# Optimization experiments

Hardware: AMD Instinct MI355X
Metric: run time of the kernel (lower is better)

Reference implementation:

```python
import jax, jax.numpy as jnp
import numpy as np

DIM = 4096
N_HEADS = 32
N_KV_HEADS = 8
HEAD_DIM = 128
ROPE_BASE = 10000.0
B, L = 4, 1024
NEG_INF = -1e9


def rope_traditional(x, base=ROPE_BASE, offset=0):
    # x: [B, H, L, Dh]; rotates interleaved pairs (x[...,2i], x[...,2i+1])
    Dh = x.shape[-1]
    Lx = x.shape[2]
    inv_freq = base ** (-jnp.arange(0, Dh, 2, dtype=jnp.float32) / Dh)  # [Dh/2]
    pos = jnp.arange(offset, offset + Lx, dtype=jnp.float32)
    ang = pos[:, None] * inv_freq  # [L, Dh/2]
    cos, sin = jnp.cos(ang), jnp.sin(ang)
    x1, x2 = x[..., ::2], x[..., 1::2]
    r1 = x1 * cos - x2 * sin
    r2 = x1 * sin + x2 * cos
    return jnp.stack([r1, r2], axis=-1).reshape(x.shape).astype(x.dtype)


def setup_inputs() -> dict:
    key = jax.random.key(0)
    ks = jax.random.split(key, 5)
    x = jax.random.normal(ks[0], (B, L, DIM), dtype=jnp.float32)
    # additive causal mask: 0 on/below diag, -inf-like above
    mask = jnp.where(jnp.tril(jnp.ones((L, L), dtype=bool)), 0.0, NEG_INF).astype(jnp.float32)
    wq = jax.random.normal(ks[1], (DIM, N_HEADS * HEAD_DIM), dtype=jnp.float32) * 0.02
    wk = jax.random.normal(ks[2], (DIM, N_KV_HEADS * HEAD_DIM), dtype=jnp.float32) * 0.02
    wv = jax.random.normal(ks[3], (DIM, N_KV_HEADS * HEAD_DIM), dtype=jnp.float32) * 0.02
    wo = jax.random.normal(ks[4], (N_HEADS * HEAD_DIM, DIM), dtype=jnp.float32) * 0.02
    return {"x": x, "mask": mask, "wq": wq, "wk": wk, "wv": wv, "wo": wo}


def reference(x, mask, wq, wk, wv, wo):
    Bx, Lx, D = x.shape
    scale = HEAD_DIM ** -0.5
    repeats = N_HEADS // N_KV_HEADS
    q = (x @ wq).reshape(Bx, Lx, N_HEADS, HEAD_DIM).transpose(0, 2, 1, 3)      # [B,H,L,Dh]
    k = (x @ wk).reshape(Bx, Lx, N_KV_HEADS, HEAD_DIM).transpose(0, 2, 1, 3)   # [B,Hkv,L,Dh]
    v = (x @ wv).reshape(Bx, Lx, N_KV_HEADS, HEAD_DIM).transpose(0, 2, 1, 3)
    # GQA expansion: head h attends to kv head h % n_kv_heads (matches
    # expand_dims+repeat(axis=1)+reshape in the original)
    k = jnp.tile(k, (1, repeats, 1, 1))  # [B,H,L,Dh]
    v = jnp.tile(v, (1, repeats, 1, 1))
    # cache=None path: rope with offset 0
    q = rope_traditional(q)
    k = rope_traditional(k)
    scores = jnp.einsum("bhqd,bhkd->bhqk", q * scale, k) + mask
    probs = jax.nn.softmax(scores.astype(jnp.float32), axis=-1).astype(scores.dtype)
    out = jnp.einsum("bhqk,bhkd->bhqd", probs, v)
    out = out.transpose(0, 2, 1, 3).reshape(Bx, Lx, D)
    return out @ wo
```

## Files before the change

kernel.cpp:

```cpp
#include <hip/hip_runtime.h>
#include <stdint.h>

typedef unsigned short u16;
typedef __bf16 bf16x8 __attribute__((ext_vector_type(8)));
typedef float f32x4 __attribute__((ext_vector_type(4)));

__device__ __forceinline__ u16 f2b(float x) {
  uint32_t b = __float_as_uint(x);
  b += 0x7fff + ((b >> 16) & 1);
  return (u16)(b >> 16);
}
__device__ __forceinline__ float b2f(u16 u) {
  return __uint_as_float(((uint32_t)u) << 16);
}

#define GLD16(src, dst)                                                                  \
  __builtin_amdgcn_global_load_lds((const __attribute__((address_space(1))) void*)(src),\
                                   (__attribute__((address_space(3))) void*)(dst), 16, 0, 0)

__device__ __forceinline__ f32x4 mfma16(bf16x8 a, bf16x8 b, f32x4 c) {
  return __builtin_amdgcn_mfma_f32_16x16x32_bf16(a, b, c, 0, 0, 0);
}

__global__ void k_rope_table(float2* __restrict__ tab) {
  int i = blockIdx.x * 256 + threadIdx.x;
  int l = i >> 6, d = i & 63;
  float inv = powf(10000.0f, -(float)(2 * d) / 128.0f);
  float ang = (float)l * inv;
  float s, c;
  sincosf(ang, &s, &c);
  tab[i] = make_float2(c, s);
}

__global__ void k_cast8(const float* __restrict__ src, u16* __restrict__ dst) {
  size_t i = (size_t)blockIdx.x * 256 + threadIdx.x;
  const float4* s4 = (const float4*)src;
  float4 a = s4[2 * i], b = s4[2 * i + 1];
  union { u16 u[8]; uint4 v; } o;
  o.u[0] = f2b(a.x); o.u[1] = f2b(a.y); o.u[2] = f2b(a.z); o.u[3] = f2b(a.w);
  o.u[4] = f2b(b.x); o.u[5] = f2b(b.y); o.u[6] = f2b(b.z); o.u[7] = f2b(b.w);
  ((uint4*)dst)[i] = o.v;
}

__global__ __launch_bounds__(256) void k_tcast(const float* __restrict__ src,
                                               u16* __restrict__ dst, int R, int C) {
  __shared__ u16 t[64][72];
  int tiles_c = C >> 6;
  int tr = blockIdx.x / tiles_c, tc = blockIdx.x % tiles_c;
  int tid = threadIdx.x;
  {
    int rr = tid >> 4, cv = tid & 15;
#pragma unroll
    for (int it = 0; it < 4; ++it) {
      int row = rr + it * 16;
      float4 v = *(const float4*)(src + (size_t)(tr * 64 + row) * C + tc * 64 + cv * 4);
      t[row][cv * 4 + 0] = f2b(v.x);
      t[row][cv * 4 + 1] = f2b(v.y);
      t[row][cv * 4 + 2] = f2b(v.z);
      t[row][cv * 4 + 3] = f2b(v.w);
    }
  }
  __syncthreads();
  {
    int cc = tid >> 3, g = tid & 7;
#pragma unroll
    for (int it = 0; it < 2; ++it) {
      int c = cc + it * 32;
      union { u16 u[8]; uint4 v; } o;
#pragma unroll
      for (int j = 0; j < 8; ++j) o.u[j] = t[g * 8 + j][c];
      *(uint4*)(dst + (size_t)(tc * 64 + c) * R + tr * 64 + g * 8) = o.v;
    }
  }
}

__global__ __launch_bounds__(256) void k_vtrans(const u16* __restrict__ qkv,
                                                u16* __restrict__ vrt) {
  __shared__ u16 t[64][72];
  int b = blockIdx.x >> 8;
  int tt = blockIdx.x & 255;
  int tr = tt >> 4, tc = tt & 15;
  int tid = threadIdx.x;
  {
    int rr = tid >> 3, g = tid & 7;
#pragma unroll
    for (int it = 0; it < 2; ++it) {
      int row = rr + it * 32;
      union { u16 u[8]; uint4 v; } o;
      o.v = *(const uint4*)(qkv + (size_t)(b * 1024 + tr * 64 + row) * 6144 + 5120 + tc * 64 + g * 8);
#pragma unroll
      for (int j = 0; j < 8; ++j) t[row][g * 8 + j] = o.u[j];
    }
  }
  __syncthreads();
  {
    int cc = tid >> 3, g = tid & 7;
#pragma unroll
    for (int it = 0; it < 2; ++it) {
      int c = cc + it * 32;
      union { u16 u[8]; uint4 v; } o;
#pragma unroll
      for (int j = 0; j < 8; ++j) o.u[j] = t[g * 8 + j][c];
      *(uint4*)(vrt + (size_t)(b * 1024 + tc * 64 + c) * 1024 + tr * 64 + g * 8) = o.v;
    }
  }
}

__global__ void k_rope(const u16* __restrict__ qkv, const float2* __restrict__ tab,
                       u16* __restrict__ qr, u16* __restrict__ kr) {
  int u = blockIdx.x * 256 + threadIdx.x;
  int row = u / 2560;
  int j = u - row * 2560;
  int b = row >> 10, l = row & 1023;
  const float scale = 0.08838834764831845f;
  if (j < 2048) {
    int h = j >> 6, dp = j & 63;
    uint32_t pair = *(const uint32_t*)(qkv + (size_t)row * 6144 + h * 128 + 2 * dp);
    float2 cs = tab[l * 64 + dp];
    float x1 = b2f((u16)pair), x2 = b2f((u16)(pair >> 16));
    float r1 = (x1 * cs.x - x2 * cs.y) * scale;
    float r2 = (x1 * cs.y + x2 * cs.x) * scale;
    uint32_t outw = (uint32_t)f2b(r1) | ((uint32_t)f2b(r2) << 16);
    *(uint32_t*)(qr + ((size_t)((b * 32 + h) * 1024 + l)) * 128 + 2 * dp) = outw;
  } else {
    int jj = j - 2048;
    int kh = jj >> 6, dp = jj & 63;
    uint32_t pair = *(const uint32_t*)(qkv + (size_t)row * 6144 + 4096 + kh * 128 + 2 * dp);
    float2 cs = tab[l * 64 + dp];
    float x1 = b2f((u16)pair), x2 = b2f((u16)(pair >> 16));
    float r1 = x1 * cs.x - x2 * cs.y;
    float r2 = x1 * cs.y + x2 * cs.x;
    uint32_t outw = (uint32_t)f2b(r1) | ((uint32_t)f2b(r2) << 16);
    *(uint32_t*)(kr + ((size_t)((b * 8 + kh) * 1024 + l)) * 128 + 2 * dp) = outw;
  }
}


#define STAGE2(s0, s1, koff, ldsoff)          \
  GLD16((s0) + (koff), dst0 + (ldsoff));      \
  GLD16((s1) + (koff), dst1 + (ldsoff));

#define LOADB(base, kh)                                                   \
  bfr[0] = *(const bf16x8*)((base) + (kh) * 8192 + 0 * 512);              \
  bfr[1] = *(const bf16x8*)((base) + (kh) * 8192 + 1 * 512);              \
  bfr[2] = *(const bf16x8*)((base) + (kh) * 8192 + 2 * 512);              \
  bfr[3] = *(const bf16x8*)((base) + (kh) * 8192 + 3 * 512);

#define LOADA(base, kh, mh)                                               \
  afr[0] = *(const bf16x8*)((base) + (kh) * 8192 + (mh) * 2048 + 0 * 512);\
  afr[1] = *(const bf16x8*)((base) + (kh) * 8192 + (mh) * 2048 + 1 * 512);\
  afr[2] = *(const bf16x8*)((base) + (kh) * 8192 + (mh) * 2048 + 2 * 512);\
  afr[3] = *(const bf16x8*)((base) + (kh) * 8192 + (mh) * 2048 + 3 * 512);

#define PH_TAIL(mh)                                                       \
  __builtin_amdgcn_sched_barrier(0);                                      \
  __builtin_amdgcn_s_barrier();                                           \
  asm volatile("s_waitcnt lgkmcnt(0)" ::: "memory");                      \
  __builtin_amdgcn_sched_barrier(0);                                      \
  __builtin_amdgcn_s_setprio(1);                                          \
  _Pragma("unroll") for (int mm = 0; mm < 4; ++mm)                        \
    _Pragma("unroll") for (int n_ = 0; n_ < 4; ++n_)                      \
      acc[(mh) * 4 + mm][n_] = mfma16(afr[mm], bfr[n_], acc[(mh) * 4 + mm][n_]); \
  __builtin_amdgcn_s_setprio(0);                                          \
  __builtin_amdgcn_sched_barrier(0);                                      \
  __builtin_amdgcn_s_barrier();

template <typename OutT>
__global__ __launch_bounds__(512, 2) void k_gemm8(const u16* __restrict__ A,
                                                  const u16* __restrict__ Bt,
                                                  OutT* __restrict__ C,
                                                  int M, int N, int K) {
  extern __shared__ u16 lds[];
  const int tid = threadIdx.x;
  const int lane = tid & 63, wid = tid >> 6;
  const int l16 = lane & 15, lhi = lane >> 4;
  const int wm = wid >> 2, wn = wid & 3;

  const int nbn = N >> 8;
  int bid = blockIdx.x;
  const int cpx = gridDim.x >> 3;
  bid = (bid & 7) * cpx + (bid >> 3);
  const int bm = (bid / nbn) << 8;
  const int bn = (bid % nbn) << 8;

  const u16* Ag = A + (size_t)bm * K;
  const u16* Bg = Bt + (size_t)bn * K;

  const int swz = (lhi ^ ((l16 >> 1) & 3)) << 3;
  const u16* pA0 = lds + wm * 4096 + l16 * 32 + swz;
  const u16* pA1 = pA0 + 32768;
  const u16* pB0 = lds + 16384 + wn * 2048 + l16 * 32 + swz;
  const u16* pB1 = pB0 + 32768;

  const int r0 = tid >> 2, g0 = tid & 3;
  const int r1 = r0 + 128;
  const size_t so0 = (size_t)r0 * K + ((g0 ^ ((r0 >> 1) & 3)) << 3);
  const size_t so1 = (size_t)r1 * K + ((g0 ^ ((r1 >> 1) & 3)) << 3);
  const u16* sA0 = Ag + so0;
  const u16* sA1 = Ag + so1;
  const u16* sB0 = Bg + so0;
  const u16* sB1 = Bg + so1;
  u16* dst0 = lds + wid * 512;
  u16* dst1 = lds + 4096 + wid * 512;

  f32x4 acc[8][4] = {};
  bf16x8 bfr[4], afr[4];

  STAGE2(sA0, sA1, 0, 0);
  STAGE2(sA0, sA1, 32, 8192);
  STAGE2(sB0, sB1, 0, 16384);
  STAGE2(sB0, sB1, 32, 24576);
  STAGE2(sB0, sB1, 64, 49152);
  STAGE2(sA0, sA1, 64, 32768);
  STAGE2(sB0, sB1, 96, 57344);
  asm volatile("s_waitcnt vmcnt(6)" ::: "memory");
  __builtin_amdgcn_s_barrier();

  const int nt = K >> 6;
  for (int t = 0; t < nt; t += 2) {
    const bool more = (t + 2) < nt;
    const int kA1 = (t + 1) * 64 + 32;
    const int k2 = (t + 2) * 64;
    const int k3 = (t + 3) * 64;
    LOADB(pB0, 0)
    LOADA(pA0, 0, 0)
    STAGE2(sA0, sA1, kA1, 40960);
    PH_TAIL(0)
    LOADA(pA0, 0, 1)
    if (more) { STAGE2(sB0, sB1, k2, 16384); }
    PH_TAIL(1)
    LOADB(pB0, 1)
    LOADA(pA0, 1, 0)
    if (more) { STAGE2(sA0, sA1, k2, 0); }
    PH_TAIL(0)
    LOADA(pA0, 1, 1)
    if (more) {
      STAGE2(sB0, sB1, k2 + 32, 24576);
      asm volatile("s_waitcnt vmcnt(6)" ::: "memory");
    } else {
      asm volatile("s_waitcnt vmcnt(0)" ::: "memory");
    }
    PH_TAIL(1)
    LOADB(pB1, 0)
    LOADA(pA1, 0, 0)
    if (more) { STAGE2(sA0, sA1, k2 + 32, 8192); }
    PH_TAIL(0)
    LOADA(pA1, 0, 1)
    if (more) { STAGE2(sB0, sB1, k3, 49152); }
    PH_TAIL(1)
    LOADB(pB1, 1)
    LOADA(pA1, 1, 0)
    if (more) { STAGE2(sA0, sA1, k3, 32768); }
    PH_TAIL(0)
    LOADA(pA1, 1, 1)
    if (more) {
      STAGE2(sB0, sB1, k3 + 32, 57344);
      asm volatile("s_waitcnt vmcnt(6)" ::: "memory");
    }
    PH_TAIL(1)
  }

#pragma unroll
  for (int m = 0; m < 8; ++m) {
    int row = bm + wm * 128 + m * 16 + lhi * 4;
#pragma unroll
    for (int n = 0; n < 4; ++n) {
      int col = bn + wn * 64 + n * 16 + l16;
#pragma unroll
      for (int r = 0; r < 4; ++r) {
        float v = acc[m][n][r];
        size_t idx = (size_t)(row + r) * N + col;
        if constexpr (sizeof(OutT) == 2) C[idx] = f2b(v);
        else C[idx] = v;
      }
    }
  }
}

__global__ __launch_bounds__(512) void k_attn(const u16* __restrict__ qr,
                                              const u16* __restrict__ kr,
                                              const u16* __restrict__ vrt,
                                              u16* __restrict__ ao) {
  __shared__ u16 Klds[8192];
  __shared__ u16 Vlds[8192];
  __shared__ u16 Plds[9216];
  int bid = blockIdx.x;
  int qb = bid & 7, h = (bid >> 3) & 31, b = bid >> 8;
  int kvh = h & 7;
  int lane = threadIdx.x & 63, w = threadIdx.x >> 6;
  int l16 = lane & 15, lhi = lane >> 4;
  int qmin = qb * 128 + w * 16;

  const u16* qbase = qr + ((size_t)((b * 32 + h) * 1024) + qmin + l16) * 128;
  bf16x8 aq[4];
#pragma unroll
  for (int kc = 0; kc < 4; ++kc) aq[kc] = *(const bf16x8*)(qbase + kc * 32 + lhi * 8);

  const u16* Kg = kr + (size_t)(b * 8 + kvh) * (1024 * 128);
  const u16* Vg = vrt + (size_t)(b * 8 + kvh) * (128 * 1024);

  float m_run[4] = {-1e30f, -1e30f, -1e30f, -1e30f};
  float l_run[4] = {0.f, 0.f, 0.f, 0.f};
  f32x4 o[8] = {};

  int nkb = 2 * qb + 2;
  for (int kb = 0; kb < nkb; ++kb) {
    int kv0 = kb * 64;
#pragma unroll
    for (int i = 0; i < 2; ++i) {
      int c = w * 128 + i * 64 + lane;
      int krow = c >> 4, g = c & 15;
      GLD16(Kg + (size_t)(kv0 + krow) * 128 + ((g ^ (krow & 7)) * 8),
            Klds + (w * 128 + i * 64) * 8);
    }
#pragma unroll
    for (int i = 0; i < 2; ++i) {
      int c = w * 128 + i * 64 + lane;
      int d = c >> 3, g = c & 7;
      GLD16(Vg + (size_t)d * 1024 + kv0 + ((g ^ (d & 7)) * 8),
            Vlds + (w * 128 + i * 64) * 8);
    }
    __syncthreads();

    f32x4 s[4] = {};
#pragma unroll
    for (int kc = 0; kc < 4; ++kc) {
#pragma unroll
      for (int n = 0; n < 4; ++n) {
        int kv = n * 16 + l16;
        int g = kc * 4 + lhi;
        bf16x8 bk = *(const bf16x8*)(Klds + kv * 128 + ((g ^ (kv & 7)) * 8));
        s[n] = mfma16(aq[kc], bk, s[n]);
      }
    }
    if (kv0 + 63 > qmin) {
#pragma unroll
      for (int n = 0; n < 4; ++n)
#pragma unroll
        for (int r = 0; r < 4; ++r) {
          int q = qmin + lhi * 4 + r;
          int kv = kv0 + n * 16 + l16;
          if (kv > q) s[n][r] = -1e30f;
        }
    }
    float pr[4][4];
#pragma unroll
    for (int r = 0; r < 4; ++r) {
      float mx = fmaxf(fmaxf(s[0][r], s[1][r]), fmaxf(s[2][r], s[3][r]));
      mx = fmaxf(mx, __shfl_xor(mx, 1));
      mx = fmaxf(mx, __shfl_xor(mx, 2));
      mx = fmaxf(mx, __shfl_xor(mx, 4));
      mx = fmaxf(mx, __shfl_xor(mx, 8));
      float mn = fmaxf(m_run[r], mx);
      float sf = __expf(m_run[r] - mn);
      m_run[r] = mn;
      float sum = 0.f;
#pragma unroll
      for (int n = 0; n < 4; ++n) {
        float p = __expf(s[n][r] - mn);
        pr[n][r] = p;
        sum += p;
      }
      sum += __shfl_xor(sum, 1);
      sum += __shfl_xor(sum, 2);
      sum += __shfl_xor(sum, 4);
      sum += __shfl_xor(sum, 8);
      l_run[r] = l_run[r] * sf + sum;
#pragma unroll
      for (int nd = 0; nd < 8; ++nd) o[nd][r] *= sf;
    }
    u16* pw = Plds + w * 1152;
#pragma unroll
    for (int n = 0; n < 4; ++n)
#pragma unroll
      for (int r = 0; r < 4; ++r) pw[(lhi * 4 + r) * 72 + n * 16 + l16] = f2b(pr[n][r]);
#pragma unroll
    for (int kc = 0; kc < 2; ++kc) {
      bf16x8 ap = *(const bf16x8*)(pw + l16 * 72 + kc * 32 + lhi * 8);
#pragma unroll
      for (int nd = 0; nd < 8; ++nd) {
        int d = nd * 16 + l16;
        int g = kc * 4 + lhi;
        bf16x8 bv = *(const bf16x8*)(Vlds + d * 64 + ((g ^ (d & 7)) * 8));
        o[nd] = mfma16(ap, bv, o[nd]);
      }
    }
    __syncthreads();
  }
#pragma unroll
  for (int r = 0; r < 4; ++r) {
    float inv = 1.0f / l_run[r];
    int q = qmin + lhi * 4 + r;
    u16* orow = ao + ((size_t)(b * 1024 + q)) * 4096 + h * 128;
#pragma unroll
    for (int nd = 0; nd < 8; ++nd) orow[nd * 16 + l16] = f2b(o[nd][r] * inv);
  }
}

extern "C" void kernel_launch(void* const* d_in, const int* in_sizes, int n_in,
                              void* d_out, int out_size, void* d_ws, size_t ws_size,
                              hipStream_t stream) {
  const float* x = (const float*)d_in[0];
  const float* wq = (const float*)d_in[2];
  const float* wk = (const float*)d_in[3];
  const float* wv = (const float*)d_in[4];
  const float* wo = (const float*)d_in[5];

  char* ws = (char*)d_ws;
  u16* xb = (u16*)(ws + 0);
  u16* wcat = (u16*)(ws + 33554432);
  u16* qr = (u16*)(ws + 0);
  u16* kr = (u16*)(ws + 33554432);
  u16* vrt = (u16*)(ws + 41943040);
  u16* ao = (u16*)(ws + 50331648);
  u16* wob = (u16*)(ws + 83886080);
  float2* tab = (float2*)(ws + 117440512);
  u16* qkv = (u16*)d_out;

  hipFuncSetAttribute((const void*)k_gemm8<u16>,
                      hipFuncAttributeMaxDynamicSharedMemorySize, 131072);
  hipFuncSetAttribute((const void*)k_gemm8<float>,
                      hipFuncAttributeMaxDynamicSharedMemorySize, 131072);

  k_rope_table<<<256, 256, 0, stream>>>(tab);
  k_cast8<<<8192, 256, 0, stream>>>(x, xb);
  k_tcast<<<4096, 256, 0, stream>>>(wq, wcat, 4096, 4096);
  k_tcast<<<1024, 256, 0, stream>>>(wk, wcat + (size_t)4096 * 4096, 4096, 1024);
  k_tcast<<<1024, 256, 0, stream>>>(wv, wcat + (size_t)5120 * 4096, 4096, 1024);
  k_tcast<<<4096, 256, 0, stream>>>(wo, wob, 4096, 4096);
  k_gemm8<u16><<<384, 512, 131072, stream>>>(xb, wcat, qkv, 4096, 6144, 4096);
  k_rope<<<40960, 256, 0, stream>>>(qkv, tab, qr, kr);
  k_vtrans<<<1024, 256, 0, stream>>>(qkv, vrt);
  k_attn<<<1024, 512, 0, stream>>>(qr, kr, vrt, ao);
  k_gemm8<float><<<256, 512, 131072, stream>>>(ao, wob, (float*)d_out, 4096, 4096, 4096);
}
```

Baseline: 561.6 us.

## Double-buffer LDS-to-register fragments to overlap ds_reads with MFMA phases

The GEMM main loop now uses two sets of A/B register fragments, so the LDS reads for the next MFMA phase are issued right after the current phase's MFMAs instead of before them. One of the two barriers per phase is removed, leaving a single barrier at the end of each phase. This is meant to hide LDS read latency behind matrix math. It costs extra VGPRs under launch_bounds(512,2), which could cause spills, and changes the ordering between LDS refills and reads, which needs the barrier placement to be correct.

```diff
diff --git a/kernel.cpp b/kernel.cpp
--- a/kernel.cpp
+++ b/kernel.cpp
@@ -140,30 +140,29 @@
   GLD16((s0) + (koff), dst0 + (ldsoff));      \
   GLD16((s1) + (koff), dst1 + (ldsoff));
 
-#define LOADB(base, kh)                                                   \
-  bfr[0] = *(const bf16x8*)((base) + (kh) * 8192 + 0 * 512);              \
-  bfr[1] = *(const bf16x8*)((base) + (kh) * 8192 + 1 * 512);              \
-  bfr[2] = *(const bf16x8*)((base) + (kh) * 8192 + 2 * 512);              \
-  bfr[3] = *(const bf16x8*)((base) + (kh) * 8192 + 3 * 512);
-
-#define LOADA(base, kh, mh)                                               \
-  afr[0] = *(const bf16x8*)((base) + (kh) * 8192 + (mh) * 2048 + 0 * 512);\
-  afr[1] = *(const bf16x8*)((base) + (kh) * 8192 + (mh) * 2048 + 1 * 512);\
-  afr[2] = *(const bf16x8*)((base) + (kh) * 8192 + (mh) * 2048 + 2 * 512);\
-  afr[3] = *(const bf16x8*)((base) + (kh) * 8192 + (mh) * 2048 + 3 * 512);
-
-#define PH_TAIL(mh)                                                       \
-  __builtin_amdgcn_sched_barrier(0);                                      \
-  __builtin_amdgcn_s_barrier();                                           \
+#define LOADB(dst, base, kh)                                              \
+  dst[0] = *(const bf16x8*)((base) + (kh) * 8192 + 0 * 512);              \
+  dst[1] = *(const bf16x8*)((base) + (kh) * 8192 + 1 * 512);              \
+  dst[2] = *(const bf16x8*)((base) + (kh) * 8192 + 2 * 512);              \
+  dst[3] = *(const bf16x8*)((base) + (kh) * 8192 + 3 * 512);
+
+#define LOADA(dst, base, kh, mh)                                          \
+  dst[0] = *(const bf16x8*)((base) + (kh) * 8192 + (mh) * 2048 + 0 * 512);\
+  dst[1] = *(const bf16x8*)((base) + (kh) * 8192 + (mh) * 2048 + 1 * 512);\
+  dst[2] = *(const bf16x8*)((base) + (kh) * 8192 + (mh) * 2048 + 2 * 512);\
+  dst[3] = *(const bf16x8*)((base) + (kh) * 8192 + (mh) * 2048 + 3 * 512);
+
+#define MFMA_PHASE(mh, AF, BF)                                            \
   asm volatile("s_waitcnt lgkmcnt(0)" ::: "memory");                      \
   __builtin_amdgcn_sched_barrier(0);                                      \
   __builtin_amdgcn_s_setprio(1);                                          \
   _Pragma("unroll") for (int mm = 0; mm < 4; ++mm)                        \
     _Pragma("unroll") for (int n_ = 0; n_ < 4; ++n_)                      \
-      acc[(mh) * 4 + mm][n_] = mfma16(afr[mm], bfr[n_], acc[(mh) * 4 + mm][n_]); \
+      acc[(mh) * 4 + mm][n_] = mfma16(AF[mm], BF[n_], acc[(mh) * 4 + mm][n_]); \
   __builtin_amdgcn_s_setprio(0);                                          \
-  __builtin_amdgcn_sched_barrier(0);                                      \
-  __builtin_amdgcn_s_barrier();
+  __builtin_amdgcn_sched_barrier(0);
+
+#define ENDP __builtin_amdgcn_s_barrier();
 
 template <typename OutT>
 __global__ __launch_bounds__(512, 2) void k_gemm8(const u16* __restrict__ A,
@@ -204,7 +203,7 @@
   u16* dst1 = lds + 4096 + wid * 512;
 
   f32x4 acc[8][4] = {};
-  bf16x8 bfr[4], afr[4];
+  bf16x8 afrA[4], afrB[4], bfrA[4], bfrB[4];
 
   STAGE2(sA0, sA1, 0, 0);
   STAGE2(sA0, sA1, 32, 8192);
@@ -215,6 +214,8 @@
   STAGE2(sB0, sB1, 96, 57344);
   asm volatile("s_waitcnt vmcnt(6)" ::: "memory");
   __builtin_amdgcn_s_barrier();
+  LOADB(bfrA, pB0, 0)
+  LOADA(afrA, pA0, 0, 0)
 
   const int nt = K >> 6;
   for (int t = 0; t < nt; t += 2) {
@@ -222,42 +223,50 @@
     const int kA1 = (t + 1) * 64 + 32;
     const int k2 = (t + 2) * 64;
     const int k3 = (t + 3) * 64;
-    LOADB(pB0, 0)
-    LOADA(pA0, 0, 0)
+    MFMA_PHASE(0, afrA, bfrA)
+    LOADA(afrB, pA0, 0, 1)
     STAGE2(sA0, sA1, kA1, 40960);
-    PH_TAIL(0)
-    LOADA(pA0, 0, 1)
+    ENDP
+    MFMA_PHASE(1, afrB, bfrA)
+    LOADB(bfrB, pB0, 1)
+    LOADA(afrA, pA0, 1, 0)
     if (more) { STAGE2(sB0, sB1, k2, 16384); }
-    PH_TAIL(1)
-    LOADB(pB0, 1)
-    LOADA(pA0, 1, 0)
+    ENDP
+    MFMA_PHASE(0, afrA, bfrB)
+    LOADA(afrB, pA0, 1, 1)
     if (more) { STAGE2(sA0, sA1, k2, 0); }
-    PH_TAIL(0)
-    LOADA(pA0, 1, 1)
+    ENDP
+    MFMA_PHASE(1, afrB, bfrB)
     if (more) {
       STAGE2(sB0, sB1, k2 + 32, 24576);
       asm volatile("s_waitcnt vmcnt(6)" ::: "memory");
     } else {
       asm volatile("s_waitcnt vmcnt(0)" ::: "memory");
     }
-    PH_TAIL(1)
-    LOADB(pB1, 0)
-    LOADA(pA1, 0, 0)
+    LOADB(bfrA, pB1, 0)
+    LOADA(afrA, pA1, 0, 0)
+    ENDP
+    MFMA_PHASE(0, afrA, bfrA)
+    LOADA(afrB, pA1, 0, 1)
     if (more) { STAGE2(sA0, sA1, k2 + 32, 8192); }
-    PH_TAIL(0)
-    LOADA(pA1, 0, 1)
+    ENDP
+    MFMA_PHASE(1, afrB, bfrA)
+    LOADB(bfrB, pB1, 1)
+    LOADA(afrA, pA1, 1, 0)
     if (more) { STAGE2(sB0, sB1, k3, 49152); }
-    PH_TAIL(1)
-    LOADB(pB1, 1)
-    LOADA(pA1, 1, 0)
+    ENDP
+    MFMA_PHASE(0, afrA, bfrB)
+    LOADA(afrB, pA1, 1, 1)
     if (more) { STAGE2(sA0, sA1, k3, 32768); }
-    PH_TAIL(0)
-    LOADA(pA1, 1, 1)
+    ENDP
+    MFMA_PHASE(1, afrB, bfrB)
     if (more) {
       STAGE2(sB0, sB1, k3 + 32, 57344);
       asm volatile("s_waitcnt vmcnt(6)" ::: "memory");
-    }
-    PH_TAIL(1)
+      LOADB(bfrA, pB0, 0)
+      LOADA(afrA, pA0, 0, 0)
+    }
+    ENDP
   }
 
 #pragma unroll
```

New measurement: 892.3 us. +58.9%, slower.
